# Kernel optimization log

Hardware: AMD Instinct MI355X
Metric: run time of the kernel (lower is better)

The kernel has to match this reference:

```python
import jax, jax.numpy as jnp
import numpy as np

VOCAB = 1_000_000
EMBED_DIM = 128
BATCH = 16_384
NOISE_COUNT = 16


def setup_inputs() -> dict:
    key = jax.random.key(0)
    k1, k2, k3, k4, k5, k6 = jax.random.split(key, 6)
    embed = jax.random.uniform(k1, (EMBED_DIM, VOCAB), jnp.float32, -1.0, 1.0)
    bias = jax.random.uniform(k2, (VOCAB, 1), jnp.float32, -1.0, 1.0)
    u = jax.random.uniform(k3, (VOCAB,), jnp.float32, 1e-3, 1.0)
    freq = u / u.sum()  # normalized unigram^0.75 noise distribution
    targets = jax.random.randint(k4, (BATCH,), 0, VOCAB)
    contexts = jax.random.randint(k5, (BATCH,), 0, VOCAB)
    noises = jax.random.randint(k6, (BATCH * NOISE_COUNT,), 0, VOCAB)
    return {"embed": embed, "bias": bias, "freq": freq,
            "targets": targets, "contexts": contexts, "noises": noises,
            "noise_count": NOISE_COUNT}


def reference(embed, bias, freq, targets, contexts, noises, noise_count):
    # embed: (E, V); bias: (V, 1); freq: (V,)
    E = embed.shape[0]
    B = targets.shape[0]
    re = 10.0
    q = embed[:, targets]                      # (E, B) target embeddings
    r = embed[:, contexts]                     # (E, B) context embeddings
    b = bias[targets, 0][None, :]              # (1, B)
    s = ((r * q).sum(0)[None, :] + b) / E      # (1, B) scaled score
    # positive term: log(sigmoid(s - log(k * p(target))))
    pos = jax.nn.log_sigmoid(s - jnp.log(noise_count * freq[targets]))
    loss = pos.sum()
    # noise term: log(1 - sigmoid(tile(s,k) - log(k * p(noise)))) = log_sigmoid(-x)
    s_tiled = jnp.tile(s, (1, noise_count))    # (1, B*k) == torch.cat((s,)*k, dim=1)
    noise_loss = jax.nn.log_sigmoid(-(s_tiled - jnp.log(noise_count * freq[noises]))).sum()
    total_loss = -(loss + noise_loss) / B
    penalty = re * ((q * q).sum() + (r * r).sum()) / (E * B)
    return total_loss + penalty
```

## Files before the change

### kernel.cpp

```cpp
#include <hip/hip_runtime.h>
#include <math.h>


__device__ __forceinline__ float log_sigmoid_f(float x) {
    return fminf(x, 0.0f) - log1pf(expf(-fabsf(x)));
}

__global__ __launch_bounds__(256) void nce_pairs_kernel(
    const float* __restrict__ embed,
    const float* __restrict__ bias,
    const float* __restrict__ freq,
    const int*   __restrict__ targets,
    const int*   __restrict__ contexts,
    const int*   __restrict__ noises,
    float*       __restrict__ block_partials,
    int V, int E, int B, int NC)
{
    __shared__ float wave_part[4];
    const int wave = threadIdx.x >> 6;
    const int lane = threadIdx.x & 63;
    const int waves_total = gridDim.x * 4;

    float acc = 0.0f;

    for (int j = blockIdx.x * 4 + wave; j < B; j += waves_total) {
        const int t = targets[j];
        const int c = contexts[j];

        float dot = 0.0f, sq = 0.0f;
        for (int e = lane; e < E; e += 64) {
            float qe = embed[(size_t)e * V + t];
            float re = embed[(size_t)e * V + c];
            dot = fmaf(qe, re, dot);
            sq  = fmaf(qe, qe, fmaf(re, re, sq));
        }
        #pragma unroll
        for (int off = 32; off > 0; off >>= 1) {
            dot += __shfl_xor(dot, off, 64);
            sq  += __shfl_xor(sq,  off, 64);
        }

        const float s = (dot + bias[t]) / (float)E;

        float term = 0.0f;
        if (lane == 0) {
            term = log_sigmoid_f(s - logf((float)NC * freq[t]));
        }
        for (int k = lane; k < NC; k += 64) {
            const int nidx = noises[j + (size_t)k * B];
            term += log_sigmoid_f(-(s - logf((float)NC * freq[nidx])));
        }
        #pragma unroll
        for (int off = 32; off > 0; off >>= 1) {
            term += __shfl_xor(term, off, 64);
        }

        if (lane == 0) {
            acc += -term / (float)B + 10.0f * sq / (float)(E * (size_t)B);
        }
    }

    if (lane == 0) wave_part[wave] = acc;
    __syncthreads();
    if (threadIdx.x == 0) {
        block_partials[blockIdx.x] =
            wave_part[0] + wave_part[1] + wave_part[2] + wave_part[3];
    }
}

__global__ __launch_bounds__(256) void reduce_partials_kernel(
    const float* __restrict__ parts, int n, float* __restrict__ out)
{
    __shared__ double sh[256];
    double a = 0.0;
    for (int i = threadIdx.x; i < n; i += 256) a += (double)parts[i];
    sh[threadIdx.x] = a;
    __syncthreads();
    for (int s = 128; s > 0; s >>= 1) {
        if (threadIdx.x < s) sh[threadIdx.x] += sh[threadIdx.x + s];
        __syncthreads();
    }
    if (threadIdx.x == 0) out[0] = (float)sh[0];
}

extern "C" void kernel_launch(void* const* d_in, const int* in_sizes, int n_in,
                              void* d_out, int out_size, void* d_ws, size_t ws_size,
                              hipStream_t stream) {
    const float* embed    = (const float*)d_in[0];
    const float* bias     = (const float*)d_in[1];
    const float* freq     = (const float*)d_in[2];
    const int*   targets  = (const int*)d_in[3];
    const int*   contexts = (const int*)d_in[4];
    const int*   noises   = (const int*)d_in[5];

    const int V  = in_sizes[2];
    const int E  = in_sizes[0] / V;
    const int B  = in_sizes[3];
    const int NC = in_sizes[5] / B;

    float* partials = (float*)d_ws;

    int nblocks = (B + 3) / 4;
    if (nblocks > 4096) nblocks = 4096;

    nce_pairs_kernel<<<nblocks, 256, 0, stream>>>(
        embed, bias, freq, targets, contexts, noises, partials, V, E, B, NC);

    reduce_partials_kernel<<<1, 256, 0, stream>>>(
        partials, nblocks, (float*)d_out);
}
```

Baseline: 101.0 us.

## Map lanes to pairs and split embedding dim across thread groups

Changes the work mapping from one wavefront per pair, with 64 lanes each reading strided embedding rows, to 32 pairs per block, with 8 thread groups each covering a contiguous E/8 slice. Partial dot and square sums are combined through shared memory instead of wave shuffles. The noise terms are also spread across the groups. This raises per-thread memory-level parallelism via unrolled loads and removes the per-pair wave reductions. The cost is extra block syncs, and only 32 distinct columns are gathered per row access, so each load is still a scattered single-float gather. The E/8 split assumes E is divisible by GSPLIT.

```diff
diff --git a/kernel.cpp b/kernel.cpp
--- a/kernel.cpp
+++ b/kernel.cpp
@@ -1,12 +1,15 @@
 #include <hip/hip_runtime.h>
 #include <math.h>
 
+
+#define PAIRS 32
+#define GSPLIT 8
 
 __device__ __forceinline__ float log_sigmoid_f(float x) {
     return fminf(x, 0.0f) - log1pf(expf(-fabsf(x)));
 }
 
-__global__ __launch_bounds__(256) void nce_pairs_kernel(
+__global__ __launch_bounds__(256) void nce_kernel(
     const float* __restrict__ embed,
     const float* __restrict__ bias,
     const float* __restrict__ freq,
@@ -16,55 +19,77 @@
     float*       __restrict__ block_partials,
     int V, int E, int B, int NC)
 {
-    __shared__ float wave_part[4];
-    const int wave = threadIdx.x >> 6;
-    const int lane = threadIdx.x & 63;
-    const int waves_total = gridDim.x * 4;
+    __shared__ float sh_dot[GSPLIT][PAIRS];
+    __shared__ float sh_sq [GSPLIT][PAIRS];
+    __shared__ float sh_s  [PAIRS];
+    __shared__ float sh_pp [PAIRS];
+    __shared__ float sh_n  [GSPLIT][PAIRS];
 
-    float acc = 0.0f;
+    const int p = threadIdx.x & (PAIRS - 1);
+    const int g = threadIdx.x >> 5;
+    const int j = blockIdx.x * PAIRS + p;
+    const bool valid = (j < B);
 
-    for (int j = blockIdx.x * 4 + wave; j < B; j += waves_total) {
+    float dot = 0.0f, sq = 0.0f;
+    if (valid) {
         const int t = targets[j];
         const int c = contexts[j];
-
-        float dot = 0.0f, sq = 0.0f;
-        for (int e = lane; e < E; e += 64) {
-            float qe = embed[(size_t)e * V + t];
-            float re = embed[(size_t)e * V + c];
+        const int epc = E / GSPLIT;
+        const int e0  = g * epc;
+        const float* ct = embed + t;
+        const float* cc = embed + c;
+        #pragma unroll 8
+        for (int e = e0; e < e0 + epc; ++e) {
+            float qe = ct[(size_t)e * V];
+            float re = cc[(size_t)e * V];
             dot = fmaf(qe, re, dot);
             sq  = fmaf(qe, qe, fmaf(re, re, sq));
         }
+    }
+    sh_dot[g][p] = dot;
+    sh_sq [g][p] = sq;
+    __syncthreads();
+
+    if (threadIdx.x < PAIRS) {
+        const int jp = blockIdx.x * PAIRS + threadIdx.x;
+        float d = 0.0f, s2 = 0.0f;
         #pragma unroll
-        for (int off = 32; off > 0; off >>= 1) {
-            dot += __shfl_xor(dot, off, 64);
-            sq  += __shfl_xor(sq,  off, 64);
+        for (int gg = 0; gg < GSPLIT; ++gg) {
+            d  += sh_dot[gg][threadIdx.x];
+            s2 += sh_sq [gg][threadIdx.x];
         }
+        float sval = 0.0f, pp = 0.0f;
+        if (jp < B) {
+            const int t = targets[jp];
+            sval = (d + bias[t]) / (float)E;
+            const float pos = log_sigmoid_f(sval - logf((float)NC * freq[t]));
+            pp = -pos / (float)B + 10.0f * s2 / ((float)E * (float)B);
+        }
+        sh_s [threadIdx.x] = sval;
+        sh_pp[threadIdx.x] = pp;
+    }
+    __syncthreads();
 
-        const float s = (dot + bias[t]) / (float)E;
-
-        float term = 0.0f;
-        if (lane == 0) {
-            term = log_sigmoid_f(s - logf((float)NC * freq[t]));
-        }
-        for (int k = lane; k < NC; k += 64) {
-            const int nidx = noises[j + (size_t)k * B];
-            term += log_sigmoid_f(-(s - logf((float)NC * freq[nidx])));
-        }
-        #pragma unroll
-        for (int off = 32; off > 0; off >>= 1) {
-            term += __shfl_xor(term, off, 64);
-        }
-
-        if (lane == 0) {
-            acc += -term / (float)B + 10.0f * sq / (float)(E * (size_t)B);
+    float nacc = 0.0f;
+    if (valid) {
+        const float sval = sh_s[p];
+        for (int k = g; k < NC; k += GSPLIT) {
+            const int n = noises[j + (size_t)k * B];
+            nacc += log_sigmoid_f(-(sval - logf((float)NC * freq[n])));
         }
     }
+    sh_n[g][p] = nacc;
+    __syncthreads();
 
-    if (lane == 0) wave_part[wave] = acc;
-    __syncthreads();
-    if (threadIdx.x == 0) {
-        block_partials[blockIdx.x] =
-            wave_part[0] + wave_part[1] + wave_part[2] + wave_part[3];
+    if (threadIdx.x < PAIRS) {
+        float a = sh_pp[threadIdx.x];
+        float nsum = 0.0f;
+        #pragma unroll
+        for (int gg = 0; gg < GSPLIT; ++gg) nsum += sh_n[gg][threadIdx.x];
+        a += -nsum / (float)B;
+        #pragma unroll
+        for (int off = 16; off > 0; off >>= 1) a += __shfl_xor(a, off, 64);
+        if (threadIdx.x == 0) block_partials[blockIdx.x] = a;
     }
 }
 
@@ -100,10 +125,9 @@
 
     float* partials = (float*)d_ws;
 
-    int nblocks = (B + 3) / 4;
-    if (nblocks > 4096) nblocks = 4096;
+    const int nblocks = (B + PAIRS - 1) / PAIRS;
 
-    nce_pairs_kernel<<<nblocks, 256, 0, stream>>>(
+    nce_kernel<<<nblocks, 256, 0, stream>>>(
         embed, bias, freq, targets, contexts, noises, partials, V, E, B, NC);
 
     reduce_partials_kernel<<<1, 256, 0, stream>>>(
```

After: 90.98 us. 1.11x faster.
